# Kernel optimization log

Measured on AMD Instinct MI355X. Metric: run time of the kernel, lower is better.

## Reference

```python
import jax, jax.numpy as jnp
import numpy as np

N, E, M, C = 4000, 60000, 16, 64        # nodes, edges, (lmax+1)^2, sphere_channels
H, HEADS, A, VC, CE, Z = 64, 8, 8, 8, 32, 90  # attn hidden, heads, alpha ch, value ch, edge ch, max elements


def _params(key):
    ks = jax.random.split(key, 10)
    g = lambda k, sh, fan: jax.random.normal(k, sh, dtype=jnp.float32) / np.float32(np.sqrt(fan))
    return [g(ks[0], (Z, CE), CE),          # emb_s: source atom embedding
            g(ks[1], (Z, CE), CE),          # emb_t: target atom embedding
            g(ks[2], (CE,), 1.0),           # w_d : distance projection
            g(ks[3], (CE, H), CE),          # We  : edge scalar -> hidden (m=0 inject)
            g(ks[4], (C, H), C),            # Ws  : source channel mix
            g(ks[5], (C, H), C),            # Wt  : target channel mix
            g(ks[6], (H, HEADS * A), H),    # Wa  : alpha features
            g(ks[7], (HEADS, A), A),        # va  : per-head alpha vector
            g(ks[8], (H, HEADS * VC), H),   # Wv  : values
            g(ks[9], (HEADS * VC, 1), HEADS * VC)]  # Wo : output proj (1 channel)


def setup_inputs() -> dict:
    key = jax.random.key(0)
    ks = jax.random.split(key, 8)
    x = jax.random.normal(ks[0], (N, M, C), dtype=jnp.float32)
    atomic_numbers = jax.random.randint(ks[1], (N,), 0, Z)
    edge_distance = jax.random.uniform(ks[2], (E,), dtype=jnp.float32) * 5.0 + 0.5
    edge_index = jax.random.randint(ks[3], (2, E), 0, N)
    noise_mask = jax.random.randint(ks[4], (N,), 0, 2).astype(bool)
    # per-edge SO3/Wigner rotation: random orthogonal [E, M, M]
    rng = np.random.default_rng(0)
    q, _ = np.linalg.qr(rng.standard_normal((E, M, M)).astype(np.float32))
    wigner = jnp.asarray(q, dtype=jnp.float32)
    names = ['emb_s', 'emb_t', 'w_d', 'We', 'Ws', 'Wt', 'Wa', 'va', 'Wv', 'Wo']
    inp = {'x': x, 'atomic_numbers': atomic_numbers, 'edge_distance': edge_distance,
           'edge_index': edge_index, 'noise_mask': noise_mask, 'wigner': wigner}
    for n, v in zip(names, _params(ks[5])):
        inp['fs_' + n] = v
    for n, v in zip(names, _params(ks[6])):
        inp['dn_' + n] = v
    return inp


def _block(x, zn, dist, src, dst, D, emb_s, emb_t, w_d, We, Ws, Wt, Wa, va, Wv, Wo):
    # gather + rotate edge-wise node features into edge-aligned frame
    xs = jnp.einsum('emn,enc->emc', D, x[src])            # [E,M,C]
    xt = jnp.einsum('emn,enc->emc', D, x[dst])            # [E,M,C]
    # scalar edge embedding (distance + source/target atom embeddings)
    e = jax.nn.silu(dist[:, None] * w_d + emb_s[zn[src]] + emb_t[zn[dst]])  # [E,CE]
    # SO2-style channel mixing; inject edge scalars into the m=0 (invariant) row
    f = jnp.einsum('emc,ch->emh', xs, Ws) + jnp.einsum('emc,ch->emh', xt, Wt)  # [E,M,H]
    f = f.at[:, 0, :].add(e @ We)
    # attention logits from the invariant part
    a = jax.nn.leaky_relu(f[:, 0, :] @ Wa, 0.2).reshape(E, HEADS, A)
    logits = jnp.einsum('eha,ha->eh', a, va)              # [E,HEADS]
    # segment softmax over incoming edges per target node
    mx = jax.ops.segment_max(logits, dst, num_segments=N)
    ex = jnp.exp(logits - mx[dst])
    alpha = ex / (jax.ops.segment_sum(ex, dst, num_segments=N)[dst] + 1e-9)
    # values, attention-weight, rotate back (D^T), scatter to nodes
    v = (f @ Wv).reshape(E, M, HEADS, VC) * alpha[:, None, :, None]
    v = jnp.einsum('emn,emhv->enhv', D, v).reshape(E, M, HEADS * VC)
    out = jax.ops.segment_sum(v, dst, num_segments=N) @ Wo  # [N,M,1]
    return out[:, 1:4, 0]  # narrow(1, 1, 3) -> l=1 vector components [N,3]


def reference(x, atomic_numbers, edge_distance, edge_index, noise_mask, wigner,
              fs_emb_s, fs_emb_t, fs_w_d, fs_We, fs_Ws, fs_Wt, fs_Wa, fs_va, fs_Wv, fs_Wo,
              dn_emb_s, dn_emb_t, dn_w_d, dn_We, dn_Ws, dn_Wt, dn_Wa, dn_va, dn_Wv, dn_Wo):
    src, dst = edge_index[0], edge_index[1]
    forces = _block(x, atomic_numbers, edge_distance, src, dst, wigner,
                    fs_emb_s, fs_emb_t, fs_w_d, fs_We, fs_Ws, fs_Wt, fs_Wa, fs_va, fs_Wv, fs_Wo)
    den = _block(x, atomic_numbers, edge_distance, src, dst, wigner,
                 dn_emb_s, dn_emb_t, dn_w_d, dn_We, dn_Ws, dn_Wt, dn_Wa, dn_va, dn_Wv, dn_Wo)
    # denoising_pos_forward with noise_mask: forces = den*mask + forces*~mask
    m = noise_mask[:, None].astype(x.dtype)
    return den * m + forces * (1.0 - m)
```

## Files before the change

### kernel.cpp

```cpp
#include <hip/hip_runtime.h>

typedef unsigned short ushort_t;
typedef __attribute__((ext_vector_type(8))) short short8;
typedef __attribute__((ext_vector_type(4))) float floatx4;

constexpr int RS = 11520;

__device__ inline float bf2f(ushort_t u) {
    union { unsigned int i; float f; } v; v.i = ((unsigned int)u) << 16; return v.f;
}
__device__ inline ushort_t f2bf(float f) {
    union { float f; unsigned int i; } v; v.f = f;
    unsigned int b = v.i + 0x7FFFu + ((v.i >> 16) & 1u);
    return (ushort_t)(b >> 16);
}

__global__ __launch_bounds__(256) void k_composites(
    const float* __restrict__ Ws0, const float* __restrict__ Wt0, const float* __restrict__ We0,
    const float* __restrict__ Wa0, const float* __restrict__ Wv0, const float* __restrict__ Wo0,
    const float* __restrict__ Ws1, const float* __restrict__ Wt1, const float* __restrict__ We1,
    const float* __restrict__ Wa1, const float* __restrict__ Wv1, const float* __restrict__ Wo1,
    float* __restrict__ cmp)
{
    int task = blockIdx.x;
    int r    = blockIdx.y;
    const float* Ws = r ? Ws1 : Ws0;
    const float* Wt = r ? Wt1 : Wt0;
    const float* We = r ? We1 : We0;
    const float* Wa = r ? Wa1 : Wa0;
    const float* Wv = r ? Wv1 : Wv0;
    const float* Wo = r ? Wo1 : Wo0;
    float* base = cmp + r * RS;

    if (task == 0 || task == 1) {
        const float* L = task ? Wt : Ws;
        float* out = base + task * 4096;
        for (int idx = threadIdx.x; idx < 4096; idx += 256) {
            int c = idx >> 6, j = idx & 63;
            float a = 0.f;
            for (int k = 0; k < 64; ++k) a += L[c * 64 + k] * Wa[k * 64 + j];
            out[idx] = a;
        }
    } else if (task == 2) {
        float* out = base + 8192;
        for (int idx = threadIdx.x; idx < 2048; idx += 256) {
            int ce = idx >> 6, j = idx & 63;
            float a = 0.f;
            for (int k = 0; k < 64; ++k) a += We[ce * 64 + k] * Wa[k * 64 + j];
            out[idx] = a;
        }
    } else {
        const float* L = (task == 3) ? Ws : (task == 4) ? Wt : We;
        int rows = (task == 5) ? 32 : 64;
        float* out = base + ((task == 3) ? 10240 : (task == 4) ? 10752 : 11264);
        for (int idx = threadIdx.x; idx < rows * 8; idx += 256) {
            int c = idx >> 3, h = idx & 7;
            float a = 0.f;
            for (int k = 0; k < 64; ++k) {
                float wv = 0.f;
                #pragma unroll
                for (int aa = 0; aa < 8; ++aa) wv += Wv[k * 64 + h * 8 + aa] * Wo[h * 8 + aa];
                a += L[c * 64 + k] * wv;
            }
            out[idx] = a;
        }
    }
}

__device__ inline short8 bfragW(const float* __restrict__ W, int colBase, int kBase,
                                int q, int n) {
    short8 f;
    #pragma unroll
    for (int j = 0; j < 8; ++j)
        f[j] = (short)f2bf(W[(kBase + q * 8 + j) * 64 + colBase + n]);
    return f;
}
__device__ inline short8 bfragP(const float* __restrict__ P0, const float* __restrict__ P1,
                                int kBase, int q, int n) {
    const float* P = (n < 8) ? P0 : P1;
    int c = n & 7;
    short8 f;
    #pragma unroll
    for (int j = 0; j < 8; ++j)
        f[j] = (short)f2bf(P[(kBase + q * 8 + j) * 8 + c]);
    return f;
}

#define MFMA(a, b, c) __builtin_amdgcn_mfma_f32_16x16x32_bf16((a), (b), (c), 0, 0, 0)

__global__ __launch_bounds__(256, 2) void k_node(
    const float* __restrict__ x, const int* __restrict__ mask,
    const float* __restrict__ cmp,
    float* __restrict__ psrc, float* __restrict__ ptgt,
    ushort_t* __restrict__ srcA, ushort_t* __restrict__ tgtA,
    int N, int totWaves)
{
    int wid  = (int)((blockIdx.x * blockDim.x + threadIdx.x) >> 6);
    int lane = threadIdx.x & 63;
    int q    = lane >> 4;
    int n16  = lane & 15;

    short8 Bs0[4][2], Bs1[4][2], Bt0[4][2], Bt1[4][2];
    #pragma unroll
    for (int t = 0; t < 4; ++t) {
        #pragma unroll
        for (int kh = 0; kh < 2; ++kh) {
            Bs0[t][kh] = bfragW(cmp,             t * 16, kh * 32, q, n16);
            Bs1[t][kh] = bfragW(cmp + RS,        t * 16, kh * 32, q, n16);
            Bt0[t][kh] = bfragW(cmp + 4096,      t * 16, kh * 32, q, n16);
            Bt1[t][kh] = bfragW(cmp + RS + 4096, t * 16, kh * 32, q, n16);
        }
    }
    short8 Bp[2], Bq[2];
    #pragma unroll
    for (int kh = 0; kh < 2; ++kh) {
        Bp[kh] = bfragP(cmp + 10240, cmp + RS + 10240, kh * 32, q, n16);
        Bq[kh] = bfragP(cmp + 10752, cmp + RS + 10752, kh * 32, q, n16);
    }

    const floatx4 zero = {0.f, 0.f, 0.f, 0.f};

    for (int nd = wid; nd < N; nd += totWaves) {
        const float* xp = x + (size_t)nd * 1024 + n16 * 64 + q * 8;
        float4 v0 = *(const float4*)(xp);
        float4 v1 = *(const float4*)(xp + 4);
        float4 v2 = *(const float4*)(xp + 32);
        float4 v3 = *(const float4*)(xp + 36);
        short8 a0, a1;
        a0[0] = (short)f2bf(v0.x); a0[1] = (short)f2bf(v0.y);
        a0[2] = (short)f2bf(v0.z); a0[3] = (short)f2bf(v0.w);
        a0[4] = (short)f2bf(v1.x); a0[5] = (short)f2bf(v1.y);
        a0[6] = (short)f2bf(v1.z); a0[7] = (short)f2bf(v1.w);
        a1[0] = (short)f2bf(v2.x); a1[1] = (short)f2bf(v2.y);
        a1[2] = (short)f2bf(v2.z); a1[3] = (short)f2bf(v2.w);
        a1[4] = (short)f2bf(v3.x); a1[5] = (short)f2bf(v3.y);
        a1[6] = (short)f2bf(v3.z); a1[7] = (short)f2bf(v3.w);

        int rsel = (mask[nd] != 0);

        {
            floatx4 c0 = zero, c1 = zero, c2 = zero, c3 = zero;
            c0 = MFMA(a0, Bs0[0][0], c0); c0 = MFMA(a1, Bs0[0][1], c0);
            c1 = MFMA(a0, Bs0[1][0], c1); c1 = MFMA(a1, Bs0[1][1], c1);
            c2 = MFMA(a0, Bs0[2][0], c2); c2 = MFMA(a1, Bs0[2][1], c2);
            c3 = MFMA(a0, Bs0[3][0], c3); c3 = MFMA(a1, Bs0[3][1], c3);
            ushort_t* sp = srcA + (size_t)nd * 2048 + (q * 4) * 64 + n16;
            #pragma unroll
            for (int rr = 0; rr < 4; ++rr) {
                sp[rr * 64 +  0] = f2bf(c0[rr]);
                sp[rr * 64 + 16] = f2bf(c1[rr]);
                sp[rr * 64 + 32] = f2bf(c2[rr]);
                sp[rr * 64 + 48] = f2bf(c3[rr]);
            }
        }
        {
            floatx4 c0 = zero, c1 = zero, c2 = zero, c3 = zero;
            c0 = MFMA(a0, Bs1[0][0], c0); c0 = MFMA(a1, Bs1[0][1], c0);
            c1 = MFMA(a0, Bs1[1][0], c1); c1 = MFMA(a1, Bs1[1][1], c1);
            c2 = MFMA(a0, Bs1[2][0], c2); c2 = MFMA(a1, Bs1[2][1], c2);
            c3 = MFMA(a0, Bs1[3][0], c3); c3 = MFMA(a1, Bs1[3][1], c3);
            ushort_t* sp = srcA + (size_t)nd * 2048 + 1024 + (q * 4) * 64 + n16;
            #pragma unroll
            for (int rr = 0; rr < 4; ++rr) {
                sp[rr * 64 +  0] = f2bf(c0[rr]);
                sp[rr * 64 + 16] = f2bf(c1[rr]);
                sp[rr * 64 + 32] = f2bf(c2[rr]);
                sp[rr * 64 + 48] = f2bf(c3[rr]);
            }
        }

        {
            floatx4 c0 = zero, c1 = zero, c2 = zero, c3 = zero;
            if (rsel) {
                c0 = MFMA(a0, Bt1[0][0], c0); c0 = MFMA(a1, Bt1[0][1], c0);
                c1 = MFMA(a0, Bt1[1][0], c1); c1 = MFMA(a1, Bt1[1][1], c1);
                c2 = MFMA(a0, Bt1[2][0], c2); c2 = MFMA(a1, Bt1[2][1], c2);
                c3 = MFMA(a0, Bt1[3][0], c3); c3 = MFMA(a1, Bt1[3][1], c3);
            } else {
                c0 = MFMA(a0, Bt0[0][0], c0); c0 = MFMA(a1, Bt0[0][1], c0);
                c1 = MFMA(a0, Bt0[1][0], c1); c1 = MFMA(a1, Bt0[1][1], c1);
                c2 = MFMA(a0, Bt0[2][0], c2); c2 = MFMA(a1, Bt0[2][1], c2);
                c3 = MFMA(a0, Bt0[3][0], c3); c3 = MFMA(a1, Bt0[3][1], c3);
            }
            ushort_t* tp = tgtA + (size_t)nd * 1024 + (q * 4) * 64 + n16;
            #pragma unroll
            for (int rr = 0; rr < 4; ++rr) {
                tp[rr * 64 +  0] = f2bf(c0[rr]);
                tp[rr * 64 + 16] = f2bf(c1[rr]);
                tp[rr * 64 + 32] = f2bf(c2[rr]);
                tp[rr * 64 + 48] = f2bf(c3[rr]);
            }
        }

        {
            floatx4 cp = zero;
            cp = MFMA(a0, Bp[0], cp); cp = MFMA(a1, Bp[1], cp);
            if (q == 0) {
                int r = n16 >> 3, h = n16 & 7;
                float* pp = psrc + (size_t)nd * 48 + r * 24 + h;
                pp[0]  = cp[1];
                pp[8]  = cp[2];
                pp[16] = cp[3];
            }
            floatx4 cq = zero;
            cq = MFMA(a0, Bq[0], cq); cq = MFMA(a1, Bq[1], cq);
            if (q == 0 && (n16 >> 3) == rsel) {
                int h = n16 & 7;
                float* pp = ptgt + (size_t)nd * 24 + h;
                pp[0]  = cq[1];
                pp[8]  = cq[2];
                pp[16] = cq[3];
            }
        }
    }
}

__global__ __launch_bounds__(256) void k_logits(
    const int* __restrict__ ei, const float* __restrict__ dist,
    const int* __restrict__ zn, const int* __restrict__ mask,
    const float* __restrict__ wig, const float* __restrict__ cmp,
    const float* __restrict__ embs0, const float* __restrict__ embt0, const float* __restrict__ wd0,
    const float* __restrict__ embs1, const float* __restrict__ embt1, const float* __restrict__ wd1,
    const float* __restrict__ va0, const float* __restrict__ va1,
    const ushort_t* __restrict__ srcA, const ushort_t* __restrict__ tgtA,
    float* __restrict__ den, float* __restrict__ exb, float* __restrict__ ejb, int E)
{
    int wv = threadIdx.x >> 6, j = threadIdx.x & 63;
    int e = blockIdx.x * 4 + wv;
    if (e >= E) return;
    int src = ei[e], dst = ei[E + e];
    int r = (mask[dst] != 0);
    float d = dist[e];
    int zs = zn[src], zt = zn[dst];

    float es;
    {
        int ce = j & 31;
        float z = r ? (d * wd1[ce] + embs1[zs * 32 + ce] + embt1[zt * 32 + ce])
                    : (d * wd0[ce] + embs0[zs * 32 + ce] + embt0[zt * 32 + ce]);
        es = z / (1.f + __expf(-z));
    }

    const float* WeWa   = cmp + r * RS + 8192;
    const float* WeWvWo = cmp + r * RS + 11264;
    int h8 = j & 7;
    float f0a = 0.f, ej = 0.f;
    #pragma unroll
    for (int ce = 0; ce < 32; ++ce) {
        float ev = __shfl(es, ce, 64);
        f0a += ev * WeWa[ce * 64 + j];
        ej  += ev * WeWvWo[ce * 8 + h8];
    }

    const ushort_t* sp = srcA + (size_t)src * 2048 + r * 1024 + j;
    const ushort_t* tp = tgtA + (size_t)dst * 1024 + j;
    const float* w0 = wig + (size_t)e * 256;
    #pragma unroll
    for (int n = 0; n < 16; ++n) {
        float sv = bf2f(sp[n * 64]) + bf2f(tp[n * 64]);
        f0a += w0[n] * sv;
    }

    float la = f0a > 0.f ? f0a : 0.2f * f0a;
    float val = la * (r ? va1[j] : va0[j]);
    val += __shfl_xor(val, 1);
    val += __shfl_xor(val, 2);
    val += __shfl_xor(val, 4);
    float ex = __expf(val);
    if (h8 == 0) {
        atomicAdd(&den[dst * 8 + (j >> 3)], ex);
        exb[(size_t)e * 8 + (j >> 3)] = ex;
    }
    if (j < 8) ejb[(size_t)e * 8 + j] = ej;
}

__global__ __launch_bounds__(256) void k_scatter(
    const int* __restrict__ ei, const int* __restrict__ mask,
    const float* __restrict__ wig,
    const float* __restrict__ psrc, const float* __restrict__ ptgt,
    const float* __restrict__ exb, const float* __restrict__ ejb,
    const float* __restrict__ den, float* __restrict__ out, int E)
{
    int t = threadIdx.x;
    int g = t >> 3, h = t & 7;
    int e = blockIdx.x * 32 + g;
    if (e >= E) return;
    int src = ei[e], dst = ei[E + e];
    int r = (mask[dst] != 0);
    float alpha = exb[(size_t)e * 8 + h] / (den[dst * 8 + h] + 1e-9f);
    const float* ps = psrc + (size_t)src * 48 + r * 24;
    const float* pt = ptgt + (size_t)dst * 24;
    float s0 = alpha * (ps[h]      + pt[h]);
    float s1 = alpha * (ps[8 + h]  + pt[8 + h]);
    float s2 = alpha * (ps[16 + h] + pt[16 + h]);
    float se = alpha * ejb[(size_t)e * 8 + h];
    #pragma unroll
    for (int off = 1; off < 8; off <<= 1) {
        s0 += __shfl_xor(s0, off);
        s1 += __shfl_xor(s1, off);
        s2 += __shfl_xor(s2, off);
        se += __shfl_xor(se, off);
    }
    if (h == 0) {
        const float* w0 = wig + (size_t)e * 256;
        atomicAdd(&out[dst * 3 + 0], s0 + w0[1] * se);
        atomicAdd(&out[dst * 3 + 1], s1 + w0[2] * se);
        atomicAdd(&out[dst * 3 + 2], s2 + w0[3] * se);
    }
}

extern "C" void kernel_launch(void* const* d_in, const int* in_sizes, int n_in,
                              void* d_out, int out_size, void* d_ws, size_t ws_size,
                              hipStream_t stream) {
    const float* x    = (const float*)d_in[0];
    const int*   zn   = (const int*)d_in[1];
    const float* dist = (const float*)d_in[2];
    const int*   ei   = (const int*)d_in[3];
    const int*   mask = (const int*)d_in[4];
    const float* wig  = (const float*)d_in[5];
    const float* fs[10]; const float* dn[10];
    for (int i = 0; i < 10; ++i) { fs[i] = (const float*)d_in[6 + i]; dn[i] = (const float*)d_in[16 + i]; }

    int N = in_sizes[1];
    int E = in_sizes[2];

    float* cmp  = (float*)d_ws;
    float* den  = cmp + 2 * RS;
    float* exb  = den + (size_t)N * 8;
    float* ejb  = exb + (size_t)E * 8;
    float* psrc = ejb + (size_t)E * 8;
    float* ptgt = psrc + (size_t)N * 48;
    ushort_t* srcA = (ushort_t*)(ptgt + (size_t)N * 24);
    ushort_t* tgtA = srcA + (size_t)N * 2048;

    hipMemsetAsync(d_out, 0, (size_t)out_size * sizeof(float), stream);
    hipMemsetAsync(den, 0, (size_t)N * 8 * sizeof(float), stream);

    k_composites<<<dim3(6, 2), 256, 0, stream>>>(
        fs[4], fs[5], fs[3], fs[6], fs[8], fs[9],
        dn[4], dn[5], dn[3], dn[6], dn[8], dn[9], cmp);

    int nodeBlocks = 512;
    int totWaves = nodeBlocks * (256 / 64);
    k_node<<<nodeBlocks, 256, 0, stream>>>(x, mask, cmp, psrc, ptgt, srcA, tgtA, N, totWaves);

    k_logits<<<(E + 3) / 4, 256, 0, stream>>>(
        ei, dist, zn, mask, wig, cmp,
        fs[0], fs[1], fs[2], dn[0], dn[1], dn[2],
        fs[7], dn[7], srcA, tgtA, den, exb, ejb, E);

    k_scatter<<<(E + 31) / 32, 256, 0, stream>>>(
        ei, mask, wig, psrc, ptgt, exb, ejb, den, (float*)d_out, E);
}
```

Baseline: 260.9 us.

## Build CSR by source and destination and replace atomic edge kernels with per-node loops

Builds CSR edge lists grouped by source and by destination (histogram, single-block scan, fill), then runs per-node kernels. Source features and target features are held in registers and reused across each node's edges. Softmax denominators and outputs are accumulated without atomics in per-destination loops. This removes the per-edge re-gather of the node rows and the atomic scatter. In exchange it adds three CSR-building launches, including a serial one-block scan, and an extra bf16 per-edge intermediate buffer. Per-node loops with 64-thread blocks are serial over edges and can suffer load imbalance.

```diff
diff --git a/kernel.cpp b/kernel.cpp
--- a/kernel.cpp
+++ b/kernel.cpp
@@ -168,7 +168,6 @@
                 sp[rr * 64 + 48] = f2bf(c3[rr]);
             }
         }
-
         {
             floatx4 c0 = zero, c1 = zero, c2 = zero, c3 = zero;
             if (rsel) {
@@ -191,7 +190,6 @@
                 tp[rr * 64 + 48] = f2bf(c3[rr]);
             }
         }
-
         {
             floatx4 cp = zero;
             cp = MFMA(a0, Bp[0], cp); cp = MFMA(a1, Bp[1], cp);
@@ -215,98 +213,210 @@
     }
 }
 
-__global__ __launch_bounds__(256) void k_logits(
+__global__ __launch_bounds__(256) void k_hist(
+    const int* __restrict__ ei, int* __restrict__ cnt_s, int* __restrict__ cnt_d, int E)
+{
+    int e = blockIdx.x * 256 + threadIdx.x;
+    if (e < E) {
+        atomicAdd(&cnt_s[ei[e]], 1);
+        atomicAdd(&cnt_d[ei[E + e]], 1);
+    }
+}
+
+__global__ __launch_bounds__(256) void k_scan(
+    const int* __restrict__ cnt_s, const int* __restrict__ cnt_d,
+    int* __restrict__ base_s, int* __restrict__ base_d,
+    int* __restrict__ woff_s, int* __restrict__ woff_d, int N)
+{
+    __shared__ int part[256];
+    int tid = threadIdx.x;
+    int chunk = (N + 255) / 256;
+    for (int a = 0; a < 2; ++a) {
+        const int* cnt = a ? cnt_d : cnt_s;
+        int* base = a ? base_d : base_s;
+        int* woff = a ? woff_d : woff_s;
+        int lo = tid * chunk, hi = min(lo + chunk, N);
+        int sum = 0;
+        for (int i = lo; i < hi; ++i) sum += cnt[i];
+        part[tid] = sum;
+        __syncthreads();
+        for (int off = 1; off < 256; off <<= 1) {
+            int v = (tid >= off) ? part[tid - off] : 0;
+            __syncthreads();
+            part[tid] += v;
+            __syncthreads();
+        }
+        int run = tid ? part[tid - 1] : 0;
+        for (int i = lo; i < hi; ++i) { base[i] = run; woff[i] = run; run += cnt[i]; }
+        __syncthreads();
+    }
+}
+
+__global__ __launch_bounds__(256) void k_fill(
+    const int* __restrict__ ei, int* __restrict__ woff_s, int* __restrict__ woff_d,
+    int* __restrict__ csr_s, int* __restrict__ csr_d, int E)
+{
+    int e = blockIdx.x * 256 + threadIdx.x;
+    if (e < E) {
+        int p = atomicAdd(&woff_s[ei[e]], 1);      csr_s[p] = e;
+        int q = atomicAdd(&woff_d[ei[E + e]], 1);  csr_d[q] = e;
+    }
+}
+
+__global__ __launch_bounds__(64) void k_src(
+    const int* __restrict__ ei, const int* __restrict__ mask,
+    const float* __restrict__ wig, const ushort_t* __restrict__ srcA,
+    const int* __restrict__ base_s, const int* __restrict__ cnt_s,
+    const int* __restrict__ csr_s, ushort_t* __restrict__ f0s, int E)
+{
+    int nd = blockIdx.x;
+    int j  = threadIdx.x;
+    int num = cnt_s[nd];
+    if (num == 0) return;
+    int beg = base_s[nd];
+
+    float y0[16], y1[16];
+    const ushort_t* sp = srcA + (size_t)nd * 2048 + j;
+    #pragma unroll
+    for (int n = 0; n < 16; ++n) {
+        y0[n] = bf2f(sp[n * 64]);
+        y1[n] = bf2f(sp[1024 + n * 64]);
+    }
+
+    for (int i = 0; i < num; ++i) {
+        int e = csr_s[beg + i];
+        int dst = ei[E + e];
+        int rr = (mask[dst] != 0);
+        const float* w0 = wig + (size_t)e * 256;
+        float acc = 0.f;
+        if (rr) {
+            #pragma unroll
+            for (int n = 0; n < 16; ++n) acc += w0[n] * y1[n];
+        } else {
+            #pragma unroll
+            for (int n = 0; n < 16; ++n) acc += w0[n] * y0[n];
+        }
+        f0s[(size_t)e * 64 + j] = f2bf(acc);
+    }
+}
+
+__global__ __launch_bounds__(64) void k_dst(
     const int* __restrict__ ei, const float* __restrict__ dist,
     const int* __restrict__ zn, const int* __restrict__ mask,
     const float* __restrict__ wig, const float* __restrict__ cmp,
     const float* __restrict__ embs0, const float* __restrict__ embt0, const float* __restrict__ wd0,
     const float* __restrict__ embs1, const float* __restrict__ embt1, const float* __restrict__ wd1,
     const float* __restrict__ va0, const float* __restrict__ va1,
-    const ushort_t* __restrict__ srcA, const ushort_t* __restrict__ tgtA,
+    const ushort_t* __restrict__ tgtA, const ushort_t* __restrict__ f0s,
+    const int* __restrict__ base_d, const int* __restrict__ cnt_d,
+    const int* __restrict__ csr_d,
     float* __restrict__ den, float* __restrict__ exb, float* __restrict__ ejb, int E)
 {
-    int wv = threadIdx.x >> 6, j = threadIdx.x & 63;
-    int e = blockIdx.x * 4 + wv;
-    if (e >= E) return;
-    int src = ei[e], dst = ei[E + e];
-    int r = (mask[dst] != 0);
-    float d = dist[e];
-    int zs = zn[src], zt = zn[dst];
-
-    float es;
-    {
-        int ce = j & 31;
-        float z = r ? (d * wd1[ce] + embs1[zs * 32 + ce] + embt1[zt * 32 + ce])
-                    : (d * wd0[ce] + embs0[zs * 32 + ce] + embt0[zt * 32 + ce]);
-        es = z / (1.f + __expf(-z));
-    }
+    int nd = blockIdx.x;
+    int j  = threadIdx.x;
+    int num = cnt_d[nd];
+    if (num == 0) { if (j < 8) den[nd * 8 + j] = 0.f; return; }
+    int beg = base_d[nd];
+    int r = (mask[nd] != 0);
+
+    const float* embs = r ? embs1 : embs0;
+    const float* embt = r ? embt1 : embt0;
+    const float* wd   = r ? wd1   : wd0;
+    float vav = r ? va1[j] : va0[j];
+
+    float y[16];
+    const ushort_t* tp = tgtA + (size_t)nd * 1024 + j;
+    #pragma unroll
+    for (int n = 0; n < 16; ++n) y[n] = bf2f(tp[n * 64]);
 
     const float* WeWa   = cmp + r * RS + 8192;
     const float* WeWvWo = cmp + r * RS + 11264;
-    int h8 = j & 7;
-    float f0a = 0.f, ej = 0.f;
-    #pragma unroll
-    for (int ce = 0; ce < 32; ++ce) {
-        float ev = __shfl(es, ce, 64);
-        f0a += ev * WeWa[ce * 64 + j];
-        ej  += ev * WeWvWo[ce * 8 + h8];
-    }
-
-    const ushort_t* sp = srcA + (size_t)src * 2048 + r * 1024 + j;
-    const ushort_t* tp = tgtA + (size_t)dst * 1024 + j;
-    const float* w0 = wig + (size_t)e * 256;
-    #pragma unroll
-    for (int n = 0; n < 16; ++n) {
-        float sv = bf2f(sp[n * 64]) + bf2f(tp[n * 64]);
-        f0a += w0[n] * sv;
-    }
-
-    float la = f0a > 0.f ? f0a : 0.2f * f0a;
-    float val = la * (r ? va1[j] : va0[j]);
-    val += __shfl_xor(val, 1);
-    val += __shfl_xor(val, 2);
-    val += __shfl_xor(val, 4);
-    float ex = __expf(val);
-    if (h8 == 0) {
-        atomicAdd(&den[dst * 8 + (j >> 3)], ex);
-        exb[(size_t)e * 8 + (j >> 3)] = ex;
-    }
-    if (j < 8) ejb[(size_t)e * 8 + j] = ej;
-}
-
-__global__ __launch_bounds__(256) void k_scatter(
+    int h8 = j & 7, ce = j & 31;
+    float wa[32], wvo[32];
+    #pragma unroll
+    for (int c = 0; c < 32; ++c) wa[c]  = WeWa[c * 64 + j];
+    #pragma unroll
+    for (int c = 0; c < 32; ++c) wvo[c] = WeWvWo[c * 8 + h8];
+
+    int zt = zn[nd];
+    float wdv = wd[ce];
+    float embtv = embt[zt * 32 + ce];
+
+    float den_acc = 0.f;
+
+    for (int i = 0; i < num; ++i) {
+        int e = csr_d[beg + i];
+        int src = ei[e];
+        float d = dist[e];
+        int zs = zn[src];
+
+        float z = d * wdv + embs[zs * 32 + ce] + embtv;
+        float es = z / (1.f + __expf(-z));
+
+        float f0a = 0.f, ej = 0.f;
+        #pragma unroll
+        for (int c = 0; c < 32; ++c) {
+            float ev = __shfl(es, c, 64);
+            f0a += ev * wa[c];
+            ej  += ev * wvo[c];
+        }
+
+        const float* w0 = wig + (size_t)e * 256;
+        #pragma unroll
+        for (int n = 0; n < 16; ++n) f0a += w0[n] * y[n];
+        f0a += bf2f(f0s[(size_t)e * 64 + j]);
+
+        float la = f0a > 0.f ? f0a : 0.2f * f0a;
+        float val = la * vav;
+        val += __shfl_xor(val, 1);
+        val += __shfl_xor(val, 2);
+        val += __shfl_xor(val, 4);
+        float ex = __expf(val);
+        float exh = __shfl(ex, (j & 7) * 8);
+        den_acc += exh;
+        if (j < 8) {
+            exb[(size_t)e * 8 + j] = exh;
+            ejb[(size_t)e * 8 + j] = ej;
+        }
+    }
+    if (j < 8) den[nd * 8 + j] = den_acc;
+}
+
+__global__ __launch_bounds__(64) void k_out(
     const int* __restrict__ ei, const int* __restrict__ mask,
     const float* __restrict__ wig,
     const float* __restrict__ psrc, const float* __restrict__ ptgt,
     const float* __restrict__ exb, const float* __restrict__ ejb,
-    const float* __restrict__ den, float* __restrict__ out, int E)
-{
+    const float* __restrict__ den,
+    const int* __restrict__ base_d, const int* __restrict__ cnt_d,
+    const int* __restrict__ csr_d,
+    float* __restrict__ out, int E)
+{
+    int nd = blockIdx.x;
     int t = threadIdx.x;
-    int g = t >> 3, h = t & 7;
-    int e = blockIdx.x * 32 + g;
-    if (e >= E) return;
-    int src = ei[e], dst = ei[E + e];
-    int r = (mask[dst] != 0);
-    float alpha = exb[(size_t)e * 8 + h] / (den[dst * 8 + h] + 1e-9f);
-    const float* ps = psrc + (size_t)src * 48 + r * 24;
-    const float* pt = ptgt + (size_t)dst * 24;
-    float s0 = alpha * (ps[h]      + pt[h]);
-    float s1 = alpha * (ps[8 + h]  + pt[8 + h]);
-    float s2 = alpha * (ps[16 + h] + pt[16 + h]);
-    float se = alpha * ejb[(size_t)e * 8 + h];
-    #pragma unroll
-    for (int off = 1; off < 8; off <<= 1) {
-        s0 += __shfl_xor(s0, off);
-        s1 += __shfl_xor(s1, off);
-        s2 += __shfl_xor(s2, off);
-        se += __shfl_xor(se, off);
-    }
-    if (h == 0) {
-        const float* w0 = wig + (size_t)e * 256;
-        atomicAdd(&out[dst * 3 + 0], s0 + w0[1] * se);
-        atomicAdd(&out[dst * 3 + 1], s1 + w0[2] * se);
-        atomicAdd(&out[dst * 3 + 2], s2 + w0[3] * se);
-    }
+    int c = t >> 3, h = t & 7;
+    int num = cnt_d[nd];
+    int beg = base_d[nd];
+    int r = (mask[nd] != 0);
+
+    float acc = 0.f;
+    float ptv = (t < 24) ? ptgt[(size_t)nd * 24 + t] : 0.f;
+    float dv  = (t < 24) ? den[nd * 8 + h] : 1.f;
+
+    for (int i = 0; i < num; ++i) {
+        int e = csr_d[beg + i];
+        int src = ei[e];
+        float ex  = (t < 24) ? exb[(size_t)e * 8 + h] : 0.f;
+        float ejv = (t < 24) ? ejb[(size_t)e * 8 + h] : 0.f;
+        float psv = (t < 24) ? psrc[(size_t)src * 48 + r * 24 + t] : 0.f;
+        float al = ex / (dv + 1e-9f);
+        float w0c = wig[(size_t)e * 256 + 1 + c];
+        acc += al * (psv + ptv) + w0c * (al * ejv);
+    }
+    acc += __shfl_xor(acc, 1);
+    acc += __shfl_xor(acc, 2);
+    acc += __shfl_xor(acc, 4);
+    if (t < 24 && h == 0) out[nd * 3 + c] = acc;
 }
 
 extern "C" void kernel_launch(void* const* d_in, const int* in_sizes, int n_in,
@@ -330,11 +440,21 @@
     float* ejb  = exb + (size_t)E * 8;
     float* psrc = ejb + (size_t)E * 8;
     float* ptgt = psrc + (size_t)N * 48;
-    ushort_t* srcA = (ushort_t*)(ptgt + (size_t)N * 24);
+    int* cnt_s  = (int*)(ptgt + (size_t)N * 24);
+    int* cnt_d  = cnt_s + N;
+    int* base_s = cnt_d + N;
+    int* base_d = base_s + N;
+    int* woff_s = base_d + N;
+    int* woff_d = woff_s + N;
+    int* csr_s  = woff_d + N;
+    int* csr_d  = csr_s + E;
+    size_t off = (size_t)((char*)(csr_d + E) - (char*)d_ws);
+    off = (off + 15) & ~(size_t)15;
+    ushort_t* srcA = (ushort_t*)((char*)d_ws + off);
     ushort_t* tgtA = srcA + (size_t)N * 2048;
-
-    hipMemsetAsync(d_out, 0, (size_t)out_size * sizeof(float), stream);
-    hipMemsetAsync(den, 0, (size_t)N * 8 * sizeof(float), stream);
+    ushort_t* f0s  = tgtA + (size_t)N * 1024;
+
+    hipMemsetAsync(cnt_s, 0, (size_t)2 * N * sizeof(int), stream);
 
     k_composites<<<dim3(6, 2), 256, 0, stream>>>(
         fs[4], fs[5], fs[3], fs[6], fs[8], fs[9],
@@ -344,11 +464,18 @@
     int totWaves = nodeBlocks * (256 / 64);
     k_node<<<nodeBlocks, 256, 0, stream>>>(x, mask, cmp, psrc, ptgt, srcA, tgtA, N, totWaves);
 
-    k_logits<<<(E + 3) / 4, 256, 0, stream>>>(
+    k_hist<<<(E + 255) / 256, 256, 0, stream>>>(ei, cnt_s, cnt_d, E);
+    k_scan<<<1, 256, 0, stream>>>(cnt_s, cnt_d, base_s, base_d, woff_s, woff_d, N);
+    k_fill<<<(E + 255) / 256, 256, 0, stream>>>(ei, woff_s, woff_d, csr_s, csr_d, E);
+
+    k_src<<<N, 64, 0, stream>>>(ei, mask, wig, srcA, base_s, cnt_s, csr_s, f0s, E);
+
+    k_dst<<<N, 64, 0, stream>>>(
         ei, dist, zn, mask, wig, cmp,
         fs[0], fs[1], fs[2], dn[0], dn[1], dn[2],
-        fs[7], dn[7], srcA, tgtA, den, exb, ejb, E);
-
-    k_scatter<<<(E + 31) / 32, 256, 0, stream>>>(
-        ei, mask, wig, psrc, ptgt, exb, ejb, den, (float*)d_out, E);
-}
+        fs[7], dn[7], tgtA, f0s, base_d, cnt_d, csr_d, den, exb, ejb, E);
+
+    k_out<<<N, 64, 0, stream>>>(
+        ei, mask, wig, psrc, ptgt, exb, ejb, den, base_d, cnt_d, csr_d,
+        (float*)d_out, E);
+}
```

After: 321.5 us. 1.23x slower.

## Replace atomic edge scatter with CSR-by-destination fused attention per node

Applied to the files above, without the earlier changes.

Builds a CSR grouping of edges by destination (histogram, single-block scan, atomic fill) and replaces the separate logits and scatter kernels with one per-node kernel. That kernel computes logits, softmax denominator and weighted sums locally and writes each output once, with no global atomics. This removes the exb/ejb intermediate buffers, the den/out memsets and the float atomics. In exchange it adds three small preprocessing kernels, one of them a serial single-block scan, and leaves load imbalance from uneven node degrees.

```diff
diff --git a/kernel.cpp b/kernel.cpp
--- a/kernel.cpp
+++ b/kernel.cpp
@@ -168,7 +168,6 @@
                 sp[rr * 64 + 48] = f2bf(c3[rr]);
             }
         }
-
         {
             floatx4 c0 = zero, c1 = zero, c2 = zero, c3 = zero;
             if (rsel) {
@@ -191,7 +190,6 @@
                 tp[rr * 64 + 48] = f2bf(c3[rr]);
             }
         }
-
         {
             floatx4 cp = zero;
             cp = MFMA(a0, Bp[0], cp); cp = MFMA(a1, Bp[1], cp);
@@ -215,97 +213,147 @@
     }
 }
 
-__global__ __launch_bounds__(256) void k_logits(
-    const int* __restrict__ ei, const float* __restrict__ dist,
-    const int* __restrict__ zn, const int* __restrict__ mask,
+__global__ __launch_bounds__(256) void k_hist(
+    const int* __restrict__ ei, int* __restrict__ cnt_d, int E)
+{
+    int e = blockIdx.x * 256 + threadIdx.x;
+    if (e < E) atomicAdd(&cnt_d[ei[E + e]], 1);
+}
+
+__global__ __launch_bounds__(256) void k_scan(
+    const int* __restrict__ cnt_d,
+    int* __restrict__ base_d, int* __restrict__ woff_d, int N)
+{
+    __shared__ int part[256];
+    int tid = threadIdx.x;
+    int chunk = (N + 255) / 256;
+    int lo = tid * chunk, hi = min(lo + chunk, N);
+    int sum = 0;
+    for (int i = lo; i < hi; ++i) sum += cnt_d[i];
+    part[tid] = sum;
+    __syncthreads();
+    for (int off = 1; off < 256; off <<= 1) {
+        int v = (tid >= off) ? part[tid - off] : 0;
+        __syncthreads();
+        part[tid] += v;
+        __syncthreads();
+    }
+    int run = tid ? part[tid - 1] : 0;
+    for (int i = lo; i < hi; ++i) { base_d[i] = run; woff_d[i] = run; run += cnt_d[i]; }
+}
+
+__global__ __launch_bounds__(256) void k_fill(
+    const int* __restrict__ ei, int* __restrict__ woff_d,
+    int* __restrict__ cd_e, int* __restrict__ cd_src, int E)
+{
+    int e = blockIdx.x * 256 + threadIdx.x;
+    if (e < E) {
+        int s = ei[e], t = ei[E + e];
+        int q = atomicAdd(&woff_d[t], 1);
+        cd_e[q] = e; cd_src[q] = s;
+    }
+}
+
+__global__ __launch_bounds__(256) void k_attn(
+    const int* __restrict__ cd_e, const int* __restrict__ cd_src,
+    const float* __restrict__ dist, const int* __restrict__ zn,
+    const int* __restrict__ mask,
     const float* __restrict__ wig, const float* __restrict__ cmp,
     const float* __restrict__ embs0, const float* __restrict__ embt0, const float* __restrict__ wd0,
     const float* __restrict__ embs1, const float* __restrict__ embt1, const float* __restrict__ wd1,
     const float* __restrict__ va0, const float* __restrict__ va1,
     const ushort_t* __restrict__ srcA, const ushort_t* __restrict__ tgtA,
-    float* __restrict__ den, float* __restrict__ exb, float* __restrict__ ejb, int E)
-{
-    int wv = threadIdx.x >> 6, j = threadIdx.x & 63;
-    int e = blockIdx.x * 4 + wv;
-    if (e >= E) return;
-    int src = ei[e], dst = ei[E + e];
-    int r = (mask[dst] != 0);
-    float d = dist[e];
-    int zs = zn[src], zt = zn[dst];
-
-    float es;
-    {
-        int ce = j & 31;
-        float z = r ? (d * wd1[ce] + embs1[zs * 32 + ce] + embt1[zt * 32 + ce])
-                    : (d * wd0[ce] + embs0[zs * 32 + ce] + embt0[zt * 32 + ce]);
-        es = z / (1.f + __expf(-z));
-    }
-
+    const float* __restrict__ psrc, const float* __restrict__ ptgt,
+    const int* __restrict__ base_d, const int* __restrict__ cnt_d,
+    float* __restrict__ out, int N)
+{
+    int nd = blockIdx.x;
+    int num = cnt_d[nd];
+    if (num == 0) {
+        if (threadIdx.x < 3) out[nd * 3 + threadIdx.x] = 0.f;
+        return;
+    }
+    int wv = threadIdx.x >> 6;
+    int j  = threadIdx.x & 63;
+    int beg = base_d[nd];
+    int r = (mask[nd] != 0);
+
+    const float* embs = r ? embs1 : embs0;
+    const float* embt = r ? embt1 : embt0;
+    const float* wd   = r ? wd1   : wd0;
+    float vav = r ? va1[j] : va0[j];
     const float* WeWa   = cmp + r * RS + 8192;
     const float* WeWvWo = cmp + r * RS + 11264;
-    int h8 = j & 7;
-    float f0a = 0.f, ej = 0.f;
+
+    int ce = j & 31, h8 = j & 7;
+    int zt = zn[nd];
+    float wdv = wd[ce];
+    float embtv = embt[zt * 32 + ce];
+
+    float y[16];
+    const ushort_t* tp = tgtA + (size_t)nd * 1024 + j;
     #pragma unroll
-    for (int ce = 0; ce < 32; ++ce) {
-        float ev = __shfl(es, ce, 64);
-        f0a += ev * WeWa[ce * 64 + j];
-        ej  += ev * WeWvWo[ce * 8 + h8];
-    }
-
-    const ushort_t* sp = srcA + (size_t)src * 2048 + r * 1024 + j;
-    const ushort_t* tp = tgtA + (size_t)dst * 1024 + j;
-    const float* w0 = wig + (size_t)e * 256;
-    #pragma unroll
-    for (int n = 0; n < 16; ++n) {
-        float sv = bf2f(sp[n * 64]) + bf2f(tp[n * 64]);
-        f0a += w0[n] * sv;
-    }
-
-    float la = f0a > 0.f ? f0a : 0.2f * f0a;
-    float val = la * (r ? va1[j] : va0[j]);
-    val += __shfl_xor(val, 1);
-    val += __shfl_xor(val, 2);
-    val += __shfl_xor(val, 4);
-    float ex = __expf(val);
-    if (h8 == 0) {
-        atomicAdd(&den[dst * 8 + (j >> 3)], ex);
-        exb[(size_t)e * 8 + (j >> 3)] = ex;
-    }
-    if (j < 8) ejb[(size_t)e * 8 + j] = ej;
-}
-
-__global__ __launch_bounds__(256) void k_scatter(
-    const int* __restrict__ ei, const int* __restrict__ mask,
-    const float* __restrict__ wig,
-    const float* __restrict__ psrc, const float* __restrict__ ptgt,
-    const float* __restrict__ exb, const float* __restrict__ ejb,
-    const float* __restrict__ den, float* __restrict__ out, int E)
-{
-    int t = threadIdx.x;
-    int g = t >> 3, h = t & 7;
-    int e = blockIdx.x * 32 + g;
-    if (e >= E) return;
-    int src = ei[e], dst = ei[E + e];
-    int r = (mask[dst] != 0);
-    float alpha = exb[(size_t)e * 8 + h] / (den[dst * 8 + h] + 1e-9f);
-    const float* ps = psrc + (size_t)src * 48 + r * 24;
-    const float* pt = ptgt + (size_t)dst * 24;
-    float s0 = alpha * (ps[h]      + pt[h]);
-    float s1 = alpha * (ps[8 + h]  + pt[8 + h]);
-    float s2 = alpha * (ps[16 + h] + pt[16 + h]);
-    float se = alpha * ejb[(size_t)e * 8 + h];
-    #pragma unroll
-    for (int off = 1; off < 8; off <<= 1) {
-        s0 += __shfl_xor(s0, off);
-        s1 += __shfl_xor(s1, off);
-        s2 += __shfl_xor(s2, off);
-        se += __shfl_xor(se, off);
-    }
-    if (h == 0) {
+    for (int n = 0; n < 16; ++n) y[n] = bf2f(tp[n * 64]);
+
+    int c = j >> 3;
+    bool act = (j < 24);
+    float ptv = act ? ptgt[(size_t)nd * 24 + j] : 0.f;
+
+    float den_acc = 0.f;
+    float accP = 0.f, accW = 0.f;
+
+    for (int i = wv; i < num; i += 4) {
+        int p = beg + i;
+        int e = cd_e[p], src = cd_src[p];
+        float d = dist[e];
+
+        float z = d * wdv + embs[zn[src] * 32 + ce] + embtv;
+        float es = z / (1.f + __expf(-z));
+
+        float f0a = 0.f, ej = 0.f;
+        #pragma unroll
+        for (int cc = 0; cc < 32; ++cc) {
+            float ev = __shfl(es, cc, 64);
+            f0a += ev * WeWa[cc * 64 + j];
+            ej  += ev * WeWvWo[cc * 8 + h8];
+        }
+
+        const ushort_t* sp = srcA + (size_t)src * 2048 + r * 1024 + j;
         const float* w0 = wig + (size_t)e * 256;
-        atomicAdd(&out[dst * 3 + 0], s0 + w0[1] * se);
-        atomicAdd(&out[dst * 3 + 1], s1 + w0[2] * se);
-        atomicAdd(&out[dst * 3 + 2], s2 + w0[3] * se);
+        #pragma unroll
+        for (int n = 0; n < 16; ++n) f0a += w0[n] * (bf2f(sp[n * 64]) + y[n]);
+
+        float la = f0a > 0.f ? f0a : 0.2f * f0a;
+        float val = la * vav;
+        val += __shfl_xor(val, 1);
+        val += __shfl_xor(val, 2);
+        val += __shfl_xor(val, 4);
+        float ex = __expf(val);
+        float exh = __shfl(ex, (j & 7) * 8);
+        if (j < 8) den_acc += exh;
+        if (act) {
+            float psv = psrc[(size_t)src * 48 + r * 24 + j];
+            accP += exh * (psv + ptv);
+            accW += w0[1 + c] * exh * ej;
+        }
+    }
+
+    __shared__ float sden[4][8];
+    __shared__ float sP[4][24];
+    __shared__ float sW[4][24];
+    if (j < 8) sden[wv][j] = den_acc;
+    if (act) { sP[wv][j] = accP; sW[wv][j] = accW; }
+    __syncthreads();
+    if (wv == 0 && act) {
+        int hh = j & 7;
+        float P = sP[0][j] + sP[1][j] + sP[2][j] + sP[3][j];
+        float W = sW[0][j] + sW[1][j] + sW[2][j] + sW[3][j];
+        float dn = sden[0][hh] + sden[1][hh] + sden[2][hh] + sden[3][hh];
+        float v = (P + W) / (dn + 1e-9f);
+        v += __shfl_xor(v, 1);
+        v += __shfl_xor(v, 2);
+        v += __shfl_xor(v, 4);
+        if (hh == 0) out[nd * 3 + c] = v;
     }
 }
 
@@ -325,16 +373,19 @@
     int E = in_sizes[2];
 
     float* cmp  = (float*)d_ws;
-    float* den  = cmp + 2 * RS;
-    float* exb  = den + (size_t)N * 8;
-    float* ejb  = exb + (size_t)E * 8;
-    float* psrc = ejb + (size_t)E * 8;
+    float* psrc = cmp + 2 * RS;
     float* ptgt = psrc + (size_t)N * 48;
-    ushort_t* srcA = (ushort_t*)(ptgt + (size_t)N * 24);
+    int* cnt_d  = (int*)(ptgt + (size_t)N * 24);
+    int* base_d = cnt_d + N;
+    int* woff_d = base_d + N;
+    int* cd_e   = woff_d + N;
+    int* cd_src = cd_e + E;
+    size_t off = (size_t)((char*)(cd_src + E) - (char*)d_ws);
+    off = (off + 15) & ~(size_t)15;
+    ushort_t* srcA = (ushort_t*)((char*)d_ws + off);
     ushort_t* tgtA = srcA + (size_t)N * 2048;
 
-    hipMemsetAsync(d_out, 0, (size_t)out_size * sizeof(float), stream);
-    hipMemsetAsync(den, 0, (size_t)N * 8 * sizeof(float), stream);
+    hipMemsetAsync(cnt_d, 0, (size_t)N * sizeof(int), stream);
 
     k_composites<<<dim3(6, 2), 256, 0, stream>>>(
         fs[4], fs[5], fs[3], fs[6], fs[8], fs[9],
@@ -344,11 +395,13 @@
     int totWaves = nodeBlocks * (256 / 64);
     k_node<<<nodeBlocks, 256, 0, stream>>>(x, mask, cmp, psrc, ptgt, srcA, tgtA, N, totWaves);
 
-    k_logits<<<(E + 3) / 4, 256, 0, stream>>>(
-        ei, dist, zn, mask, wig, cmp,
+    k_hist<<<(E + 255) / 256, 256, 0, stream>>>(ei, cnt_d, E);
+    k_scan<<<1, 256, 0, stream>>>(cnt_d, base_d, woff_d, N);
+    k_fill<<<(E + 255) / 256, 256, 0, stream>>>(ei, woff_d, cd_e, cd_src, E);
+
+    k_attn<<<N, 256, 0, stream>>>(
+        cd_e, cd_src, dist, zn, mask, wig, cmp,
         fs[0], fs[1], fs[2], dn[0], dn[1], dn[2],
-        fs[7], dn[7], srcA, tgtA, den, exb, ejb, E);
-
-    k_scatter<<<(E + 31) / 32, 256, 0, stream>>>(
-        ei, mask, wig, psrc, ptgt, exb, ejb, den, (float*)d_out, E);
-}
+        fs[7], dn[7], srcA, tgtA, psrc, ptgt, base_d, cnt_d,
+        (float*)d_out, N);
+}
```

New measurement: 333.5 us. 27.9% more time.

## Sort edges by source node and swizzle logits blocks across XCDs

Applied to the files above, without the earlier changes.

Adds a counting sort of edges by source node (histogram, scan and fill kernels), so k_logits handles edges sharing a source together and reuses that node's srcA rows from cache. The block index is remapped so that each group of 8 interleaved blocks maps to contiguous chunks, which appears aimed at keeping one source's edges on the same XCD/L2. The two memsets are folded into an extra task of k_composites. This costs three extra kernel launches plus atomics, and the atomic fill makes the edge order within each source nondeterministic.

```diff
diff --git a/kernel.cpp b/kernel.cpp
--- a/kernel.cpp
+++ b/kernel.cpp
@@ -20,10 +20,20 @@
     const float* __restrict__ Wa0, const float* __restrict__ Wv0, const float* __restrict__ Wo0,
     const float* __restrict__ Ws1, const float* __restrict__ Wt1, const float* __restrict__ We1,
     const float* __restrict__ Wa1, const float* __restrict__ Wv1, const float* __restrict__ Wo1,
-    float* __restrict__ cmp)
+    float* __restrict__ cmp, float* __restrict__ den, int* __restrict__ cnt_s,
+    float* __restrict__ out, int N)
 {
     int task = blockIdx.x;
     int r    = blockIdx.y;
+    if (task == 6) {
+        if (r == 0) {
+            for (int i = threadIdx.x; i < N * 8; i += 256) den[i] = 0.f;
+            for (int i = threadIdx.x; i < N; i += 256) cnt_s[i] = 0;
+        } else {
+            for (int i = threadIdx.x; i < N * 3; i += 256) out[i] = 0.f;
+        }
+        return;
+    }
     const float* Ws = r ? Ws1 : Ws0;
     const float* Wt = r ? Wt1 : Wt0;
     const float* We = r ? We1 : We0;
@@ -34,25 +44,25 @@
 
     if (task == 0 || task == 1) {
         const float* L = task ? Wt : Ws;
-        float* out = base + task * 4096;
+        float* outp = base + task * 4096;
         for (int idx = threadIdx.x; idx < 4096; idx += 256) {
             int c = idx >> 6, j = idx & 63;
             float a = 0.f;
             for (int k = 0; k < 64; ++k) a += L[c * 64 + k] * Wa[k * 64 + j];
-            out[idx] = a;
+            outp[idx] = a;
         }
     } else if (task == 2) {
-        float* out = base + 8192;
+        float* outp = base + 8192;
         for (int idx = threadIdx.x; idx < 2048; idx += 256) {
             int ce = idx >> 6, j = idx & 63;
             float a = 0.f;
             for (int k = 0; k < 64; ++k) a += We[ce * 64 + k] * Wa[k * 64 + j];
-            out[idx] = a;
+            outp[idx] = a;
         }
     } else {
         const float* L = (task == 3) ? Ws : (task == 4) ? Wt : We;
         int rows = (task == 5) ? 32 : 64;
-        float* out = base + ((task == 3) ? 10240 : (task == 4) ? 10752 : 11264);
+        float* outp = base + ((task == 3) ? 10240 : (task == 4) ? 10752 : 11264);
         for (int idx = threadIdx.x; idx < rows * 8; idx += 256) {
             int c = idx >> 3, h = idx & 7;
             float a = 0.f;
@@ -62,7 +72,7 @@
                 for (int aa = 0; aa < 8; ++aa) wv += Wv[k * 64 + h * 8 + aa] * Wo[h * 8 + aa];
                 a += L[c * 64 + k] * wv;
             }
-            out[idx] = a;
+            outp[idx] = a;
         }
     }
 }
@@ -168,7 +178,6 @@
                 sp[rr * 64 + 48] = f2bf(c3[rr]);
             }
         }
-
         {
             floatx4 c0 = zero, c1 = zero, c2 = zero, c3 = zero;
             if (rsel) {
@@ -191,7 +200,6 @@
                 tp[rr * 64 + 48] = f2bf(c3[rr]);
             }
         }
-
         {
             floatx4 cp = zero;
             cp = MFMA(a0, Bp[0], cp); cp = MFMA(a1, Bp[1], cp);
@@ -215,20 +223,65 @@
     }
 }
 
+__global__ __launch_bounds__(256) void k_hist(
+    const int* __restrict__ ei, int* __restrict__ cnt_s, int E)
+{
+    int e = blockIdx.x * 256 + threadIdx.x;
+    if (e < E) atomicAdd(&cnt_s[ei[e]], 1);
+}
+
+__global__ __launch_bounds__(256) void k_scan(
+    const int* __restrict__ cnt_s, int* __restrict__ woff_s, int N)
+{
+    __shared__ int part[256];
+    int tid = threadIdx.x;
+    int chunk = (N + 255) / 256;
+    int lo = tid * chunk, hi = min(lo + chunk, N);
+    int sum = 0;
+    for (int i = lo; i < hi; ++i) sum += cnt_s[i];
+    part[tid] = sum;
+    __syncthreads();
+    for (int off = 1; off < 256; off <<= 1) {
+        int v = (tid >= off) ? part[tid - off] : 0;
+        __syncthreads();
+        part[tid] += v;
+        __syncthreads();
+    }
+    int run = tid ? part[tid - 1] : 0;
+    for (int i = lo; i < hi; ++i) { woff_s[i] = run; run += cnt_s[i]; }
+}
+
+__global__ __launch_bounds__(256) void k_fill(
+    const int* __restrict__ ei, int* __restrict__ woff_s,
+    int* __restrict__ cs_e, int* __restrict__ cs_src, int* __restrict__ cs_dst, int E)
+{
+    int e = blockIdx.x * 256 + threadIdx.x;
+    if (e < E) {
+        int s = ei[e], t = ei[E + e];
+        int p = atomicAdd(&woff_s[s], 1);
+        cs_e[p] = e; cs_src[p] = s; cs_dst[p] = t;
+    }
+}
+
 __global__ __launch_bounds__(256) void k_logits(
-    const int* __restrict__ ei, const float* __restrict__ dist,
-    const int* __restrict__ zn, const int* __restrict__ mask,
+    const int* __restrict__ cs_e, const int* __restrict__ cs_src,
+    const int* __restrict__ cs_dst,
+    const float* __restrict__ dist, const int* __restrict__ zn,
+    const int* __restrict__ mask,
     const float* __restrict__ wig, const float* __restrict__ cmp,
     const float* __restrict__ embs0, const float* __restrict__ embt0, const float* __restrict__ wd0,
     const float* __restrict__ embs1, const float* __restrict__ embt1, const float* __restrict__ wd1,
     const float* __restrict__ va0, const float* __restrict__ va1,
     const ushort_t* __restrict__ srcA, const ushort_t* __restrict__ tgtA,
-    float* __restrict__ den, float* __restrict__ exb, float* __restrict__ ejb, int E)
+    float* __restrict__ den, float* __restrict__ exb, float* __restrict__ ejb,
+    int E, int B8)
 {
     int wv = threadIdx.x >> 6, j = threadIdx.x & 63;
-    int e = blockIdx.x * 4 + wv;
-    if (e >= E) return;
-    int src = ei[e], dst = ei[E + e];
+    int b = blockIdx.x;
+    int chunk = (b & 7) * B8 + (b >> 3);
+    int p = chunk * 4 + wv;
+    if (p >= E) return;
+    int e = cs_e[p], src = cs_src[p], dst = cs_dst[p];
     int r = (mask[dst] != 0);
     float d = dist[e];
     int zs = zn[src], zt = zn[dst];
@@ -330,24 +383,36 @@
     float* ejb  = exb + (size_t)E * 8;
     float* psrc = ejb + (size_t)E * 8;
     float* ptgt = psrc + (size_t)N * 48;
-    ushort_t* srcA = (ushort_t*)(ptgt + (size_t)N * 24);
+    int* cnt_s  = (int*)(ptgt + (size_t)N * 24);
+    int* woff_s = cnt_s + N;
+    int* cs_e   = woff_s + N;
+    int* cs_src = cs_e + E;
+    int* cs_dst = cs_src + E;
+    size_t off = (size_t)((char*)(cs_dst + E) - (char*)d_ws);
+    off = (off + 15) & ~(size_t)15;
+    ushort_t* srcA = (ushort_t*)((char*)d_ws + off);
     ushort_t* tgtA = srcA + (size_t)N * 2048;
 
-    hipMemsetAsync(d_out, 0, (size_t)out_size * sizeof(float), stream);
-    hipMemsetAsync(den, 0, (size_t)N * 8 * sizeof(float), stream);
-
-    k_composites<<<dim3(6, 2), 256, 0, stream>>>(
+    k_composites<<<dim3(7, 2), 256, 0, stream>>>(
         fs[4], fs[5], fs[3], fs[6], fs[8], fs[9],
-        dn[4], dn[5], dn[3], dn[6], dn[8], dn[9], cmp);
+        dn[4], dn[5], dn[3], dn[6], dn[8], dn[9],
+        cmp, den, cnt_s, (float*)d_out, N);
 
     int nodeBlocks = 512;
     int totWaves = nodeBlocks * (256 / 64);
     k_node<<<nodeBlocks, 256, 0, stream>>>(x, mask, cmp, psrc, ptgt, srcA, tgtA, N, totWaves);
 
-    k_logits<<<(E + 3) / 4, 256, 0, stream>>>(
-        ei, dist, zn, mask, wig, cmp,
+    k_hist<<<(E + 255) / 256, 256, 0, stream>>>(ei, cnt_s, E);
+    k_scan<<<1, 256, 0, stream>>>(cnt_s, woff_s, N);
+    k_fill<<<(E + 255) / 256, 256, 0, stream>>>(ei, woff_s, cs_e, cs_src, cs_dst, E);
+
+    int nchunks = (E + 3) / 4;
+    int B8 = (nchunks + 7) / 8;
+    int B = B8 * 8;
+    k_logits<<<B, 256, 0, stream>>>(
+        cs_e, cs_src, cs_dst, dist, zn, mask, wig, cmp,
         fs[0], fs[1], fs[2], dn[0], dn[1], dn[2],
-        fs[7], dn[7], srcA, tgtA, den, exb, ejb, E);
+        fs[7], dn[7], srcA, tgtA, den, exb, ejb, E, B8);
 
     k_scatter<<<(E + 31) / 32, 256, 0, stream>>>(
         ei, mask, wig, psrc, ptgt, exb, ejb, den, (float*)d_out, E);
```

After: 284.0 us. 1.09x slower.
